# Kernel tuning notes

Hardware: AMD Instinct MI355X
Metric: run time of the kernel (lower is better)

Reference implementation:

```python
import jax, jax.numpy as jnp
import numpy as np

B, N, C_IN = 4, 4096, 64
DIM = 64
NKP = 15
K = 32               # neighbor_limits
CONV_RADIUS = 0.1 * 2.0   # conv_radius * rigid_scale (is_deform=False)
KERNEL_RADIUS = 0.12
RECEP = 1.2          # kernel_point_receptive_radius
TRANS_DIM = 128
INF = 1000000.0


def _square_distance(src, dst):
    # src [B,N,3], dst [B,M,3] -> [B,N,M]
    d = -2.0 * jnp.einsum('bnc,bmc->bnm', src, dst)
    d = d + jnp.sum(src * src, -1)[:, :, None]
    d = d + jnp.sum(dst * dst, -1)[:, None, :]
    return d


def _query_ball(xyz, radius):
    # xyz [B,N,3] -> neighbor idx [B,N,K]; out-of-radius mapped to N (shadow)
    n = xyz.shape[1]
    sq = _square_distance(xyz, xyz)
    idx = jnp.broadcast_to(jnp.arange(n, dtype=jnp.int32), sq.shape)
    idx = jnp.where(sq > radius * radius, n, idx)
    idx = jnp.sort(idx, axis=-1)[:, :, :K]
    return idx


def _index_points(points_bcn, idx, pad_val):
    # points [B,C,N], idx [B,N,K] -> [B,N,K,C]; index N hits shadow row = pad_val
    p = jnp.transpose(points_bcn, (0, 2, 1))          # [B,N,C]
    shadow = jnp.full((p.shape[0], 1, p.shape[2]), pad_val, p.dtype)
    p = jnp.concatenate([p, shadow], axis=1)          # [B,N+1,C]
    b_idx = jnp.arange(p.shape[0])[:, None, None]
    return p[b_idx, idx]                              # [B,N,K,C]


def setup_inputs() -> dict:
    key = jax.random.key(0)
    ks = jax.random.split(key, 12)
    pos = jax.random.uniform(ks[0], (B, 3, N), dtype=jnp.float32)
    feat = jax.random.normal(ks[1], (B, C_IN, N), dtype=jnp.float32)
    # kernel points: center point at origin, rest inside kernel_radius ball ('center' mode)
    kp_rest = jax.random.uniform(ks[2], (3, NKP - 1), minval=-KERNEL_RADIUS,
                                 maxval=KERNEL_RADIUS, dtype=jnp.float32)
    kp_pos = jnp.concatenate([jnp.zeros((3, 1), jnp.float32), kp_rest], axis=1)  # [3,NKP]
    s = 0.05
    cb_w = jax.random.normal(ks[3], (DIM, C_IN), jnp.float32) * s
    cb_b = jax.random.normal(ks[4], (DIM,), jnp.float32) * s
    kp_weight = jax.random.normal(ks[5], (NKP, DIM, DIM), jnp.float32) * s
    kp_bias = jax.random.normal(ks[6], (DIM,), jnp.float32) * s
    ce_w = jax.random.normal(ks[7], (C_IN, DIM), jnp.float32) * s
    ce_b = jax.random.normal(ks[8], (C_IN,), jnp.float32) * s
    f1_w = jax.random.normal(ks[9], (2 * DIM, 2 * DIM), jnp.float32) * s
    f1_b = jnp.zeros((2 * DIM,), jnp.float32)
    f2_w = jax.random.normal(ks[10], (TRANS_DIM, 2 * DIM), jnp.float32) * s
    f2_b = jnp.zeros((TRANS_DIM,), jnp.float32)
    return dict(pos=pos, feat=feat, kp_pos=kp_pos, cb_w=cb_w, cb_b=cb_b,
                kp_weight=kp_weight, kp_bias=kp_bias, ce_w=ce_w, ce_b=ce_b,
                f1_w=f1_w, f1_b=f1_b, f2_w=f2_w, f2_b=f2_b)


def reference(pos, feat, kp_pos, cb_w, cb_b, kp_weight, kp_bias, ce_w, ce_b,
              f1_w, f1_b, f2_w, f2_b):
    xyz = jnp.transpose(jax.lax.stop_gradient(pos), (0, 2, 1))       # [B,N,3]
    neighbor_idx = _query_ball(xyz, CONV_RADIUS)                     # [B,N,K]
    # NOTE: with is_deform=False the original code does NOT subtract the center
    # position; rel_neighbor_pos is the absolute gathered positions.
    neighbor_pos = jnp.transpose(_index_points(pos, neighbor_idx, INF),
                                 (0, 3, 1, 2))                        # [B,3,N,K]
    feat0 = jnp.einsum('oc,bcn->bon', cb_w, feat) + cb_b[None, :, None]
    neighbor_feat = _index_points(feat0, neighbor_idx, 0.0)           # [B,N,K,DIM]

    kp_pos_deform = kp_pos.reshape(1, 3, 1, NKP) + 0.0                # offset = 0
    diff = neighbor_pos[..., None] - kp_pos_deform[:, :, :, None, :]  # [B,3,N,K,NKP]
    sq_d = jnp.sum(diff * diff, axis=1)                               # [B,N,K,NKP]
    w = jnp.clip(1.0 - jnp.sqrt(sq_d) / RECEP, 0.0)                   # [B,N,K,NKP]
    w = jnp.transpose(w, (0, 1, 3, 2))                                # [B,N,NKP,K]
    weighted = jnp.einsum('bnpk,bnkc->bnpc', w, neighbor_feat)        # [B,N,NKP,DIM]
    out = jnp.einsum('bnpc,pcd->bnd', weighted, kp_weight) + kp_bias  # [B,N,DIM]
    out = jax.nn.relu(jnp.transpose(out, (0, 2, 1)))                  # [B,DIM,N]
    out = jax.nn.relu(jnp.einsum('oc,bcn->bon', ce_w, out)
                      + ce_b[None, :, None] + feat)                   # [B,C_IN,N]

    fuse_in = jnp.concatenate(
        [jnp.transpose(weighted, (0, 3, 1, 2)),                       # [B,DIM,N,NKP]
         jnp.broadcast_to(out[..., None], (B, DIM, N, NKP))], axis=1) # [B,2DIM,N,NKP]
    h = jax.nn.relu(jnp.einsum('oc,bcnk->bonk', f1_w, fuse_in)
                    + f1_b[None, :, None, None])
    fuse = jax.nn.relu(jnp.einsum('oc,bcnk->bonk', f2_w, h)
                       + f2_b[None, :, None, None])                   # [B,TRANS_DIM,N,NKP]
    return out, kp_pos_deform, fuse
```

## Files before the change

kernel.cpp:

```cpp
#include <hip/hip_runtime.h>
#include <hip/hip_bf16.h>
#include <stdint.h>

#define NPTS 4096
#define NB   4
#define KNN  32
#define NKPT 15

#define OFF_IDX      0ULL
#define OFF_FEAT0    2097152ULL
#define OFF_WEIGHTED 6292480ULL
#define OFF_HO       37749760ULL
#define OFF_W1P      41944064ULL
#define OFF_W2P      41976832ULL
#define OFF_KPWP     42009600ULL

#define OUT_OFF_OUT  0
#define OUT_OFF_KP   1048576
#define OUT_OFF_FUSE 1048621

#define SBU(u) ((u) ^ (((u) >> 3) & 7))

typedef __attribute__((ext_vector_type(8))) short short8v;
typedef __attribute__((ext_vector_type(4))) float f32x4;

__device__ __forceinline__ unsigned short bf16b(float f) {
  __hip_bfloat16 h = __float2bfloat16(f);
  return *(unsigned short*)&h;
}
__device__ __forceinline__ unsigned pkbf(float lo, float hi) {
  return (unsigned)bf16b(lo) | ((unsigned)bf16b(hi) << 16);
}
__device__ __forceinline__ float bflo(unsigned u) { return __uint_as_float(u << 16); }
__device__ __forceinline__ float bfhi(unsigned u) { return __uint_as_float(u & 0xffff0000u); }

__global__ __launch_bounds__(256) void k012(const float* __restrict__ pos,
                                            const float* __restrict__ feat,
                                            const float* __restrict__ cb_w,
                                            const float* __restrict__ cb_b,
                                            const float* __restrict__ f1_w,
                                            const float* __restrict__ f2_w,
                                            const float* __restrict__ kpw,
                                            const float* __restrict__ kp_pos,
                                            int* __restrict__ idx_ws,
                                            float* __restrict__ feat0,
                                            unsigned short* __restrict__ w1p,
                                            unsigned short* __restrict__ w2p,
                                            unsigned short* __restrict__ kpwp,
                                            float* __restrict__ out_kp) {
  __shared__ float cbt[64 * 65];
  const int blk = blockIdx.x;
  if (blk < 4096) {
    const int w = threadIdx.x >> 6, lane = threadIdx.x & 63;
    const int pt = blk * 4 + w;
    const int b = pt >> 12, n = pt & 4095;
    const float* px = pos + (size_t)b * 3 * NPTS;
    const double x0 = (double)px[n], y0 = (double)px[NPTS + n], z0 = (double)px[2 * NPTS + n];
    const double ssrc = x0 * x0 + y0 * y0 + z0 * z0;
    const double RAD = 0.1 * 2.0;
    const double R2 = RAD * RAD;
    int cnt = 0;
    int* op = idx_ws + (size_t)pt * KNN;
    for (int ch = 0; ch < 64; ++ch) {
      const int j = ch * 64 + lane;
      const double xj = (double)px[j], yj = (double)px[NPTS + j], zj = (double)px[2 * NPTS + j];
      const double dot  = x0 * xj + y0 * yj + z0 * zj;
      const double sdst = xj * xj + yj * yj + zj * zj;
      const double sq = -2.0 * dot + ssrc + sdst;
      const bool keep = !(sq > R2);
      const unsigned long long m = __ballot(keep);
      if (keep) {
        const int p = cnt + (int)__popcll(m & ((1ULL << lane) - 1ULL));
        if (p < KNN) op[p] = j;
      }
      cnt += (int)__popcll(m);
      if (cnt >= KNN) break;
    }
    const int s = cnt + lane;
    if (s < KNN) op[s] = NPTS;
    return;
  }
  if (blk < 8192) {
    const int t = threadIdx.x;
    #pragma unroll
    for (int q = 0; q < 16; ++q) {
      const int idx = q * 256 + t;
      const int d = idx >> 6, c = idx & 63;
      cbt[c * 65 + d] = cb_w[idx];
    }
    __syncthreads();
    const int ptl = t >> 6, d = t & 63;
    const int pt = (blk - 4096) * 4 + ptl;
    const int b = pt >> 12, n = pt & 4095;
    const float* fp = feat + (size_t)b * 64 * NPTS + n;
    float acc = 0.f;
    #pragma unroll
    for (int c = 0; c < 64; ++c) acc = fmaf(cbt[c * 65 + d], fp[(size_t)c * NPTS], acc);
    acc += cb_b[d];
    feat0[((size_t)b * (NPTS + 1) + n) * 64 + d] = acc;
    return;
  }
  int t = (blk - 8192) * 256 + threadIdx.x;
  if (t < 32768) {
    const int w = t >> 14;
    const int i = t & 16383;
    const int j = i & 7, l = (i >> 3) & 63, kc = (i >> 9) & 3, ot = i >> 11;
    const int o = ot * 16 + (l & 15);
    const int k = kc * 32 + (l >> 4) * 8 + j;
    const float* src = w ? f2_w : f1_w;
    unsigned short* dst = w ? w2p : w1p;
    dst[i] = bf16b(src[o * 128 + k]);
    return;
  }
  t -= 32768;
  if (t < 61440) {
    const int j = t & 7, l = (t >> 3) & 63, nt = (t >> 9) & 3, kc = t >> 11;
    const int k = kc * 32 + (l >> 4) * 8 + j;
    const int d = nt * 16 + (l & 15);
    kpwp[t] = bf16b(kpw[(size_t)k * 64 + d]);
    return;
  }
  t -= 61440;
  if (t < NB * 64) { int b = t >> 6, d = t & 63; feat0[((size_t)b * (NPTS + 1) + NPTS) * 64 + d] = 0.f; return; }
  t -= NB * 64;
  if (t < 45) out_kp[t] = kp_pos[t];
}

__global__ __launch_bounds__(256) void k3_weighted(const float* __restrict__ pos,
                                                   const int* __restrict__ idx_ws,
                                                   const float* __restrict__ feat0,
                                                   const float* __restrict__ kp_pos,
                                                   unsigned short* __restrict__ wbf) {
  __shared__ int   nidx[4][KNN];
  __shared__ float npx[4][KNN], npy[4][KNN], npz[4][KNN];
  __shared__ float kp[48];
  __shared__ float wl[4][KNN * 16];
  const int wv = threadIdx.x >> 6, lane = threadIdx.x & 63;
  const int pt = blockIdx.x * 4 + wv;
  const int b = pt >> 12;
  if (threadIdx.x < 45) kp[threadIdx.x] = kp_pos[threadIdx.x];
  if (lane < KNN) {
    const int ki = idx_ws[(size_t)pt * KNN + lane];
    nidx[wv][lane] = ki;
    const bool v = ki < NPTS;
    const float* px = pos + (size_t)b * 3 * NPTS;
    npx[wv][lane] = v ? px[ki] : 1000000.0f;
    npy[wv][lane] = v ? px[NPTS + ki] : 1000000.0f;
    npz[wv][lane] = v ? px[2 * NPTS + ki] : 1000000.0f;
  }
  __syncthreads();
  #pragma unroll
  for (int r = 0; r < 8; ++r) {
    const int i = r * 64 + lane;
    const int k = i >> 4, p = i & 15;
    float wvv = 0.f;
    if (p < 15) {
      const float dx = npx[wv][k] - kp[p];
      const float dy = npy[wv][k] - kp[15 + p];
      const float dz = npz[wv][k] - kp[30 + p];
      const float d2 = dx * dx + dy * dy + dz * dz;
      wvv = fmaxf(1.0f - sqrtf(d2) / 1.2f, 0.f);
    }
    wl[wv][i] = wvv;
  }
  __syncthreads();
  float acc[16];
  #pragma unroll
  for (int p = 0; p < 16; ++p) acc[p] = 0.f;
  const float* f0 = feat0 + (size_t)b * (NPTS + 1) * 64 + lane;
  for (int k = 0; k < KNN; ++k) {
    const float f = f0[(size_t)nidx[wv][k] * 64];
    #pragma unroll
    for (int q = 0; q < 4; ++q) {
      const float4 w4 = *(const float4*)&wl[wv][k * 16 + q * 4];
      acc[q * 4 + 0] = fmaf(w4.x, f, acc[q * 4 + 0]);
      acc[q * 4 + 1] = fmaf(w4.y, f, acc[q * 4 + 1]);
      acc[q * 4 + 2] = fmaf(w4.z, f, acc[q * 4 + 2]);
      acc[q * 4 + 3] = fmaf(w4.w, f, acc[q * 4 + 3]);
    }
  }
  unsigned short* wp = wbf + (size_t)pt * NKPT * 64 + lane;
  #pragma unroll
  for (int p = 0; p < 15; ++p) wp[(size_t)p * 64] = bf16b(acc[p]);
}

__global__ __launch_bounds__(256) void k45(const unsigned short* __restrict__ wbf,
                                           const unsigned short* __restrict__ kpwp,
                                           const float* __restrict__ kp_bias,
                                           const float* __restrict__ ce_w,
                                           const float* __restrict__ ce_b,
                                           const float* __restrict__ feat,
                                           const unsigned short* __restrict__ w1p,
                                           const float* __restrict__ f1_b,
                                           float* __restrict__ out,
                                           unsigned short* __restrict__ hOb) {
  __shared__ float r0[64 * 65];
  __shared__ float cwt[64 * 64];
  __shared__ unsigned short outT[64 * 74];
  const int t = threadIdx.x;
  const int b = blockIdx.x >> 6;
  const int n0 = (blockIdx.x & 63) * 64;
  const int wv = t >> 6, lane = t & 63;
  #pragma unroll
  for (int q = 0; q < 16; ++q) {
    const int idx = q * 256 + t;
    cwt[idx] = ce_w[(idx & 63) * 64 + (idx >> 6)];
  }
  const short8v* kf = (const short8v*)kpwp;
  f32x4 acc[4];
  #pragma unroll
  for (int nt = 0; nt < 4; ++nt) acc[nt] = (f32x4){0.f, 0.f, 0.f, 0.f};
  const int m0 = b * 4096 + n0 + wv * 16;
  const unsigned short* ap = wbf + (size_t)(m0 + (lane & 15)) * 960 + (lane >> 4) * 8;
  #pragma unroll 6
  for (int kc = 0; kc < 30; ++kc) {
    const short8v a = *(const short8v*)&ap[kc * 32];
    #pragma unroll
    for (int nt = 0; nt < 4; ++nt)
      acc[nt] = __builtin_amdgcn_mfma_f32_16x16x32_bf16(a, kf[(kc * 4 + nt) * 64 + lane], acc[nt], 0, 0, 0);
  }
  const int rl = wv * 16 + (lane >> 4) * 4;
  #pragma unroll
  for (int nt = 0; nt < 4; ++nt) {
    const int d = nt * 16 + (lane & 15);
    const float bv = kp_bias[d];
    #pragma unroll
    for (int r = 0; r < 4; ++r)
      r0[(rl + r) * 65 + d] = fmaxf(acc[nt][r] + bv, 0.f);
  }
  __syncthreads();
  const int nl = t & 63, og = t >> 6;
  float facc[16];
  #pragma unroll
  for (int j = 0; j < 16; ++j) facc[j] = 0.f;
  for (int c = 0; c < 64; ++c) {
    const float x = r0[nl * 65 + c];
    #pragma unroll
    for (int q = 0; q < 4; ++q) {
      const float4 w4 = *(const float4*)&cwt[c * 64 + og * 16 + q * 4];
      facc[q * 4 + 0] = fmaf(w4.x, x, facc[q * 4 + 0]);
      facc[q * 4 + 1] = fmaf(w4.y, x, facc[q * 4 + 1]);
      facc[q * 4 + 2] = fmaf(w4.z, x, facc[q * 4 + 2]);
      facc[q * 4 + 3] = fmaf(w4.w, x, facc[q * 4 + 3]);
    }
  }
  #pragma unroll
  for (int q = 0; q < 4; ++q) {
    const float4 cb4 = *(const float4*)&ce_b[og * 16 + q * 4];
    const float cbv[4] = {cb4.x, cb4.y, cb4.z, cb4.w};
    #pragma unroll
    for (int j = 0; j < 4; ++j) {
      const int o = og * 16 + q * 4 + j;
      const float fv = feat[((size_t)b * 64 + o) * 4096 + n0 + nl];
      const float v = fmaxf((facc[q * 4 + j] + cbv[j]) + fv, 0.f);
      out[((size_t)b * 64 + o) * 4096 + n0 + nl] = v;
      outT[o * 74 + nl] = bf16b(v);
    }
  }
  __syncthreads();
  const short8v* w1f = (const short8v*)w1p;
  f32x4 hacc[8];
  #pragma unroll
  for (int ot = 0; ot < 8; ++ot) hacc[ot] = (f32x4){0.f, 0.f, 0.f, 0.f};
  const int nw = lane & 15;
  #pragma unroll
  for (int kc2 = 0; kc2 < 2; ++kc2) {
    short8v bfr;
    #pragma unroll
    for (int j = 0; j < 8; ++j)
      bfr[j] = (short)outT[(kc2 * 32 + (lane >> 4) * 8 + j) * 74 + wv * 16 + nw];
    #pragma unroll
    for (int ot = 0; ot < 8; ++ot)
      hacc[ot] = __builtin_amdgcn_mfma_f32_16x16x32_bf16(w1f[(ot * 4 + 2 + kc2) * 64 + lane], bfr, hacc[ot], 0, 0, 0);
  }
  const int rb = (lane >> 4) * 4;
  unsigned short* hp = hOb + ((size_t)b * 4096 + n0 + wv * 16 + nw) * 128;
  #pragma unroll
  for (int ot = 0; ot < 8; ++ot) {
    const int o0 = ot * 16 + rb;
    const float4 b1 = *(const float4*)&f1_b[o0];
    uint2 pk;
    pk.x = pkbf(hacc[ot][0] + b1.x, hacc[ot][1] + b1.y);
    pk.y = pkbf(hacc[ot][2] + b1.z, hacc[ot][3] + b1.w);
    *(uint2*)&hp[o0] = pk;
  }
}

__global__ __launch_bounds__(256, 2) void k6_fuse(const unsigned short* __restrict__ wbf,
                                                  const unsigned short* __restrict__ hOb,
                                                  const unsigned short* __restrict__ w1p,
                                                  const unsigned short* __restrict__ w2p,
                                                  const float* __restrict__ f2_b,
                                                  float* __restrict__ fuse) {
  __shared__ __attribute__((aligned(16))) unsigned short SB[16384];
  __shared__ __attribute__((aligned(8))) unsigned short hOS[12 * 128];
  const int t = threadIdx.x;
  const int blk = blockIdx.x;
  const int b = blk / 480;
  const int ml0 = (blk - b * 480) * 128;
  const size_t M0 = (size_t)blk * 128;
  const int wv = t >> 6, lane = t & 63;
  const short8v* w1f = (const short8v*)w1p;
  const short8v* w2f = (const short8v*)w2p;

  short8v w1r[16];
  #pragma unroll
  for (int ot = 0; ot < 8; ++ot)
    #pragma unroll
    for (int kc = 0; kc < 2; ++kc)
      w1r[ot * 2 + kc] = w1f[(ot * 4 + kc) * 64 + lane];

  #pragma unroll
  for (int q = 0; q < 4; ++q) {
    const int chunk = q * 256 + t;
    const int m = chunk >> 3, a = chunk & 7;
    const uint4 pk = *(const uint4*)&wbf[(M0 + m) * 64 + a * 8];
    const int kc = a >> 2, hi = a & 3;
    const int u = ((m >> 4) * 4 + kc) * 64 + hi * 16 + (m & 15);
    *(uint4*)&SB[SBU(u) * 8] = pk;
  }
  const int nmin = ml0 / 15;
  #pragma unroll
  for (int q = 0; q < 3; ++q) {
    const int idx = q * 256 + t;
    const int row = idx >> 6, pr = idx & 63;
    int n = nmin + row;
    if (n > 4095) n = 4095;
    ((unsigned*)hOS)[idx] = ((const unsigned*)(hOb + ((size_t)b * 4096 + n) * 128))[pr];
  }
  __syncthreads();

  short8v xf[4];
  #pragma unroll
  for (int mt = 0; mt < 2; ++mt)
    #pragma unroll
    for (int kc = 0; kc < 2; ++kc) {
      const int u = ((wv * 2 + mt) * 4 + kc) * 64 + lane;
      xf[mt * 2 + kc] = *(const short8v*)&SB[SBU(u) * 8];
    }

  const int rb = (lane >> 4) * 4;
  const int dnA = (ml0 + wv * 32 + (lane & 15)) / 15 - nmin;
  const int dnB = (ml0 + wv * 32 + 16 + (lane & 15)) / 15 - nmin;
  f32x4 acc[8][2];
  #pragma unroll
  for (int ot = 0; ot < 8; ++ot) {
    const uint2 pa = *(const uint2*)&hOS[dnA * 128 + ot * 16 + rb];
    const uint2 pb = *(const uint2*)&hOS[dnB * 128 + ot * 16 + rb];
    acc[ot][0] = (f32x4){bflo(pa.x), bfhi(pa.x), bflo(pa.y), bfhi(pa.y)};
    acc[ot][1] = (f32x4){bflo(pb.x), bfhi(pb.x), bflo(pb.y), bfhi(pb.y)};
  }
  short8v w2a[16];
  #pragma unroll
  for (int i = 0; i < 16; ++i) w2a[i] = w2f[i * 64 + lane];

  #pragma unroll
  for (int kc = 0; kc < 2; ++kc) {
    #pragma unroll
    for (int ot = 0; ot < 8; ++ot) {
      acc[ot][0] = __builtin_amdgcn_mfma_f32_16x16x32_bf16(w1r[ot * 2 + kc], xf[kc],     acc[ot][0], 0, 0, 0);
      acc[ot][1] = __builtin_amdgcn_mfma_f32_16x16x32_bf16(w1r[ot * 2 + kc], xf[2 + kc], acc[ot][1], 0, 0, 0);
    }
  }
  #pragma unroll
  for (int ot = 0; ot < 8; ++ot) {
    const int o0 = ot * 16 + rb;
    const int kc = o0 >> 5, hi = (o0 >> 3) & 3, j0 = o0 & 7;
    #pragma unroll
    for (int mt = 0; mt < 2; ++mt) {
      const f32x4 h = acc[ot][mt];
      const float h0 = fmaxf(h[0], 0.f);
      const float h1 = fmaxf(h[1], 0.f);
      const float h2 = fmaxf(h[2], 0.f);
      const float h3 = fmaxf(h[3], 0.f);
      const int u = ((wv * 2 + mt) * 4 + kc) * 64 + hi * 16 + (lane & 15);
      uint2 pk;
      pk.x = pkbf(h0, h1);
      pk.y = pkbf(h2, h3);
      *(uint2*)&SB[SBU(u) * 8 + j0] = pk;
    }
  }
  short8v w2b[16];
  #pragma unroll
  for (int i = 0; i < 16; ++i) w2b[i] = w2f[(16 + i) * 64 + lane];

  short8v hf[8];
  #pragma unroll
  for (int mt = 0; mt < 2; ++mt)
    #pragma unroll
    for (int kc = 0; kc < 4; ++kc) {
      const int u = ((wv * 2 + mt) * 4 + kc) * 64 + lane;
      hf[mt * 4 + kc] = *(const short8v*)&SB[SBU(u) * 8];
    }
  #pragma unroll
  for (int ot = 0; ot < 8; ++ot) {
    acc[ot][0] = (f32x4){0.f, 0.f, 0.f, 0.f};
    acc[ot][1] = (f32x4){0.f, 0.f, 0.f, 0.f};
  }
  #pragma unroll
  for (int kc = 0; kc < 4; ++kc) {
    #pragma unroll
    for (int ot = 0; ot < 4; ++ot) {
      acc[ot][0] = __builtin_amdgcn_mfma_f32_16x16x32_bf16(w2a[ot * 4 + kc], hf[kc],     acc[ot][0], 0, 0, 0);
      acc[ot][1] = __builtin_amdgcn_mfma_f32_16x16x32_bf16(w2a[ot * 4 + kc], hf[4 + kc], acc[ot][1], 0, 0, 0);
    }
  }
  #pragma unroll
  for (int kc = 0; kc < 4; ++kc) {
    #pragma unroll
    for (int ot = 4; ot < 8; ++ot) {
      acc[ot][0] = __builtin_amdgcn_mfma_f32_16x16x32_bf16(w2b[(ot - 4) * 4 + kc], hf[kc],     acc[ot][0], 0, 0, 0);
      acc[ot][1] = __builtin_amdgcn_mfma_f32_16x16x32_bf16(w2b[(ot - 4) * 4 + kc], hf[4 + kc], acc[ot][1], 0, 0, 0);
    }
  }
  float* fp0 = fuse + (size_t)b * 128 * 61440 + ml0 + wv * 32 + (lane & 15);
  #pragma unroll
  for (int ot = 0; ot < 8; ++ot) {
    const int o0 = ot * 16 + rb;
    const float4 b2 = *(const float4*)&f2_b[o0];
    const float bv[4] = {b2.x, b2.y, b2.z, b2.w};
    #pragma unroll
    for (int mt = 0; mt < 2; ++mt) {
      const f32x4 vacc = acc[ot][mt];
      #pragma unroll
      for (int r = 0; r < 4; ++r)
        fp0[(size_t)(o0 + r) * 61440 + mt * 16] = fmaxf(vacc[r] + bv[r], 0.f);
    }
  }
}

extern "C" void kernel_launch(void* const* d_in, const int* in_sizes, int n_in,
                              void* d_out, int out_size, void* d_ws, size_t ws_size,
                              hipStream_t stream) {
  const float* pos     = (const float*)d_in[0];
  const float* feat    = (const float*)d_in[1];
  const float* kp_pos  = (const float*)d_in[2];
  const float* cb_w    = (const float*)d_in[3];
  const float* cb_b    = (const float*)d_in[4];
  const float* kpw     = (const float*)d_in[5];
  const float* kp_bias = (const float*)d_in[6];
  const float* ce_w    = (const float*)d_in[7];
  const float* ce_b    = (const float*)d_in[8];
  const float* f1_w    = (const float*)d_in[9];
  const float* f1_b    = (const float*)d_in[10];
  const float* f2_w    = (const float*)d_in[11];
  const float* f2_b    = (const float*)d_in[12];
  float* out = (float*)d_out;
  char* ws = (char*)d_ws;
  int*   idx_ws   = (int*)(ws + OFF_IDX);
  float* feat0    = (float*)(ws + OFF_FEAT0);
  unsigned short* wbf  = (unsigned short*)(ws + OFF_WEIGHTED);
  unsigned short* hOb  = (unsigned short*)(ws + OFF_HO);
  unsigned short* w1p  = (unsigned short*)(ws + OFF_W1P);
  unsigned short* w2p  = (unsigned short*)(ws + OFF_W2P);
  unsigned short* kpwp = (unsigned short*)(ws + OFF_KPWP);

  k012<<<8562, 256, 0, stream>>>(pos, feat, cb_w, cb_b, f1_w, f2_w, kpw, kp_pos,
                                 idx_ws, feat0, w1p, w2p, kpwp, out + OUT_OFF_KP);
  k3_weighted<<<4096, 256, 0, stream>>>(pos, idx_ws, feat0, kp_pos, wbf);
  k45<<<256, 256, 0, stream>>>(wbf, kpwp, kp_bias, ce_w, ce_b, feat, w1p, f1_b,
                               out + OUT_OFF_OUT, hOb);
  k6_fuse<<<1920, 256, 0, stream>>>(wbf, hOb, w1p, w2p, f2_b, out + OUT_OFF_FUSE);
}
```

Measured before the change: 137.1 us.

## Use float ball query with double fallback, one-wave weighted blocks, nontemporal stores

The ball-query distance test now runs in fp32 and falls back to fp64 only when the squared distance lies within a small margin of the radius, so most lanes avoid slow double-precision math while keeping the same neighbor selection. The weighted-aggregation kernel is relaunched as one 64-thread block per point instead of four waves per block, which removes block-wide syncs across unrelated points. Output stores for the main output and the large fuse tensor use nontemporal hints to reduce cache pollution. The epsilon-guarded fallback could in principle differ from the all-double path when fp32 rounding error exceeds the margin.

New measurement: 216.8 us. +58.1%, slower.

```diff
diff --git a/kernel.cpp b/kernel.cpp
--- a/kernel.cpp
+++ b/kernel.cpp
@@ -55,19 +55,31 @@
     const int pt = blk * 4 + w;
     const int b = pt >> 12, n = pt & 4095;
     const float* px = pos + (size_t)b * 3 * NPTS;
-    const double x0 = (double)px[n], y0 = (double)px[NPTS + n], z0 = (double)px[2 * NPTS + n];
-    const double ssrc = x0 * x0 + y0 * y0 + z0 * z0;
+    const float x0 = px[n], y0 = px[NPTS + n], z0 = px[2 * NPTS + n];
+    const float ssrcf = x0 * x0 + y0 * y0 + z0 * z0;
+    const double x0d = (double)x0, y0d = (double)y0, z0d = (double)z0;
+    const double ssrcd = x0d * x0d + y0d * y0d + z0d * z0d;
     const double RAD = 0.1 * 2.0;
     const double R2 = RAD * RAD;
+    const float R2f = (float)R2;
     int cnt = 0;
     int* op = idx_ws + (size_t)pt * KNN;
     for (int ch = 0; ch < 64; ++ch) {
       const int j = ch * 64 + lane;
-      const double xj = (double)px[j], yj = (double)px[NPTS + j], zj = (double)px[2 * NPTS + j];
-      const double dot  = x0 * xj + y0 * yj + z0 * zj;
-      const double sdst = xj * xj + yj * yj + zj * zj;
-      const double sq = -2.0 * dot + ssrc + sdst;
-      const bool keep = !(sq > R2);
+      const float xj = px[j], yj = px[NPTS + j], zj = px[2 * NPTS + j];
+      const float dotf = x0 * xj + y0 * yj + z0 * zj;
+      const float sdf  = xj * xj + yj * yj + zj * zj;
+      const float sqf  = -2.0f * dotf + ssrcf + sdf;
+      const float diff = sqf - R2f;
+      bool keep;
+      if (__builtin_expect(fabsf(diff) <= 1e-4f, 0)) {
+        const double xd = (double)xj, yd = (double)yj, zd = (double)zj;
+        const double dd = -2.0 * (x0d * xd + y0d * yd + z0d * zd) + ssrcd
+                          + (xd * xd + yd * yd + zd * zd);
+        keep = !(dd > R2);
+      } else {
+        keep = (diff <= 0.0f);
+      }
       const unsigned long long m = __ballot(keep);
       if (keep) {
         const int p = cnt + (int)__popcll(m & ((1ULL << lane) - 1ULL));
@@ -126,42 +138,42 @@
   if (t < 45) out_kp[t] = kp_pos[t];
 }
 
-__global__ __launch_bounds__(256) void k3_weighted(const float* __restrict__ pos,
-                                                   const int* __restrict__ idx_ws,
-                                                   const float* __restrict__ feat0,
-                                                   const float* __restrict__ kp_pos,
-                                                   unsigned short* __restrict__ wbf) {
-  __shared__ int   nidx[4][KNN];
-  __shared__ float npx[4][KNN], npy[4][KNN], npz[4][KNN];
+__global__ __launch_bounds__(64) void k3_weighted(const float* __restrict__ pos,
+                                                  const int* __restrict__ idx_ws,
+                                                  const float* __restrict__ feat0,
+                                                  const float* __restrict__ kp_pos,
+                                                  unsigned short* __restrict__ wbf) {
+  __shared__ int   nidx[KNN];
+  __shared__ float npx[KNN], npy[KNN], npz[KNN];
   __shared__ float kp[48];
-  __shared__ float wl[4][KNN * 16];
-  const int wv = threadIdx.x >> 6, lane = threadIdx.x & 63;
-  const int pt = blockIdx.x * 4 + wv;
+  __shared__ float wl[KNN * 16];
+  const int lane = threadIdx.x;
+  const int pt = blockIdx.x;
   const int b = pt >> 12;
-  if (threadIdx.x < 45) kp[threadIdx.x] = kp_pos[threadIdx.x];
+  if (lane < 45) kp[lane] = kp_pos[lane];
   if (lane < KNN) {
     const int ki = idx_ws[(size_t)pt * KNN + lane];
-    nidx[wv][lane] = ki;
+    nidx[lane] = ki;
     const bool v = ki < NPTS;
     const float* px = pos + (size_t)b * 3 * NPTS;
-    npx[wv][lane] = v ? px[ki] : 1000000.0f;
-    npy[wv][lane] = v ? px[NPTS + ki] : 1000000.0f;
-    npz[wv][lane] = v ? px[2 * NPTS + ki] : 1000000.0f;
+    npx[lane] = v ? px[ki] : 1000000.0f;
+    npy[lane] = v ? px[NPTS + ki] : 1000000.0f;
+    npz[lane] = v ? px[2 * NPTS + ki] : 1000000.0f;
   }
   __syncthreads();
   #pragma unroll
   for (int r = 0; r < 8; ++r) {
     const int i = r * 64 + lane;
     const int k = i >> 4, p = i & 15;
-    float wvv = 0.f;
+    float wv = 0.f;
     if (p < 15) {
-      const float dx = npx[wv][k] - kp[p];
-      const float dy = npy[wv][k] - kp[15 + p];
-      const float dz = npz[wv][k] - kp[30 + p];
+      const float dx = npx[k] - kp[p];
+      const float dy = npy[k] - kp[15 + p];
+      const float dz = npz[k] - kp[30 + p];
       const float d2 = dx * dx + dy * dy + dz * dz;
-      wvv = fmaxf(1.0f - sqrtf(d2) / 1.2f, 0.f);
-    }
-    wl[wv][i] = wvv;
+      wv = fmaxf(1.0f - sqrtf(d2) / 1.2f, 0.f);
+    }
+    wl[i] = wv;
   }
   __syncthreads();
   float acc[16];
@@ -169,10 +181,10 @@
   for (int p = 0; p < 16; ++p) acc[p] = 0.f;
   const float* f0 = feat0 + (size_t)b * (NPTS + 1) * 64 + lane;
   for (int k = 0; k < KNN; ++k) {
-    const float f = f0[(size_t)nidx[wv][k] * 64];
+    const float f = f0[(size_t)nidx[k] * 64];
     #pragma unroll
     for (int q = 0; q < 4; ++q) {
-      const float4 w4 = *(const float4*)&wl[wv][k * 16 + q * 4];
+      const float4 w4 = *(const float4*)&wl[k * 16 + q * 4];
       acc[q * 4 + 0] = fmaf(w4.x, f, acc[q * 4 + 0]);
       acc[q * 4 + 1] = fmaf(w4.y, f, acc[q * 4 + 1]);
       acc[q * 4 + 2] = fmaf(w4.z, f, acc[q * 4 + 2]);
@@ -253,7 +265,7 @@
       const int o = og * 16 + q * 4 + j;
       const float fv = feat[((size_t)b * 64 + o) * 4096 + n0 + nl];
       const float v = fmaxf((facc[q * 4 + j] + cbv[j]) + fv, 0.f);
-      out[((size_t)b * 64 + o) * 4096 + n0 + nl] = v;
+      __builtin_nontemporal_store(v, &out[((size_t)b * 64 + o) * 4096 + n0 + nl]);
       outT[o * 74 + nl] = bf16b(v);
     }
   }
@@ -424,7 +436,8 @@
       const f32x4 vacc = acc[ot][mt];
       #pragma unroll
       for (int r = 0; r < 4; ++r)
-        fp0[(size_t)(o0 + r) * 61440 + mt * 16] = fmaxf(vacc[r] + bv[r], 0.f);
+        __builtin_nontemporal_store(fmaxf(vacc[r] + bv[r], 0.f),
+                                    &fp0[(size_t)(o0 + r) * 61440 + mt * 16]);
     }
   }
 }
@@ -457,7 +470,7 @@
 
   k012<<<8562, 256, 0, stream>>>(pos, feat, cb_w, cb_b, f1_w, f2_w, kpw, kp_pos,
                                  idx_ws, feat0, w1p, w2p, kpwp, out + OUT_OFF_KP);
-  k3_weighted<<<4096, 256, 0, stream>>>(pos, idx_ws, feat0, kp_pos, wbf);
+  k3_weighted<<<16384, 64, 0, stream>>>(pos, idx_ws, feat0, kp_pos, wbf);
   k45<<<256, 256, 0, stream>>>(wbf, kpwp, kp_bias, ce_w, ce_b, feat, w1p, f1_b,
                                out + OUT_OFF_OUT, hOb);
   k6_fuse<<<1920, 256, 0, stream>>>(wbf, hOb, w1p, w2p, f2_b, out + OUT_OFF_FUSE);
```
